# Performance work log

Hardware: AMD Instinct MI355X
Metric: run time of the kernel (lower is better)

## Reference

```python
import jax, jax.numpy as jnp
import numpy as np

ALPHA = 0.5
EPS = 1e-10

def setup_inputs() -> dict:
    key = jax.random.key(0)
    k1, k2, k3, k4 = jax.random.split(key, 4)
    B, S, H = 8, 2048, 768
    query_embs = jax.random.normal(k1, (B, S, H), dtype=jnp.float32)
    key_embs = jax.random.normal(k2, (B, S, H), dtype=jnp.float32)
    q_mask = (jax.random.uniform(k3, (B, S)) > 0.1).astype(jnp.float32)
    k_mask = (jax.random.uniform(k4, (B, S)) > 0.1).astype(jnp.float32)
    q_mask = q_mask.at[:, 0].set(1.0)
    k_mask = k_mask.at[:, 0].set(1.0)
    return {"query_embs": query_embs, "key_embs": key_embs,
            "q_mask": q_mask, "k_mask": k_mask, "gumbel_temp": 1.0}

def _l2norm(x):
    # torch F.normalize: x / max(||x||, eps-ish); use rsqrt with tiny floor
    n = jnp.sqrt(jnp.sum(x * x, axis=-1, keepdims=True))
    return x / jnp.maximum(n, 1e-12)

def reference(query_embs, key_embs, q_mask, k_mask, gumbel_temp):
    B, S, H = query_embs.shape
    q = _l2norm(query_embs)
    k = _l2norm(key_embs)
    sim = jnp.einsum('bqh,bkh->bqk', q, k)  # [B,S,S]
    # exponential distance decay w_{ij} = exp(-alpha*|i-j|)
    pos = jnp.arange(S)
    dist = jnp.abs(pos[:, None] - pos[None, :]).astype(sim.dtype)
    sim = sim * jnp.exp(-ALPHA * dist)
    valid = q_mask[:, :, None] * k_mask[:, None, :]  # [B,S,S]
    # eval path: no Gumbel noise
    noisy = sim / gumbel_temp
    noisy = noisy * valid - (1.0 - valid) * 1e9
    p = jax.nn.softmax(noisy, axis=-1)
    agg = jnp.einsum('bqk,bkh->bqh', p, k)
    scores = jnp.sum(q * agg, axis=-1) * q_mask  # [B,S]
    denom = jnp.maximum(jnp.sum(q_mask, axis=-1), 1.0)
    return jnp.sum(scores, axis=-1) / denom  # [B]
```

## Files before the change

kernel.cpp:

```cpp
#include <hip/hip_runtime.h>
#include <math.h>

#define SB 8
#define SS 2048
#define SH 768
#define ALPHA 0.5f

typedef __fp16 f16x8 __attribute__((ext_vector_type(8)));
typedef float f32x4 __attribute__((ext_vector_type(4)));

__device__ __forceinline__ float dot4(float4 a, float4 b) {
  return a.x*b.x + a.y*b.y + a.z*b.z + a.w*b.w;
}
__device__ __forceinline__ unsigned int pk2(float a, float b) {
  return __builtin_bit_cast(unsigned int, __builtin_amdgcn_cvt_pkrtz(a, b));
}
#define MFMA(a, b, c) __builtin_amdgcn_mfma_f32_16x16x32_f16(a, b, c, 0, 0, 0)


__global__ __launch_bounds__(256) void kprep_kernel(
    const float* __restrict__ K, const float* __restrict__ km,
    const float* __restrict__ qm,
    __fp16* __restrict__ Khs, float* __restrict__ ksum,
    float* __restrict__ Nk, float* __restrict__ qsum) {
  __shared__ float4 red[4][3][64];
  int b = blockIdx.y, jc = blockIdx.x, t = threadIdx.x;
  int w = t >> 6, lane = t & 63;
  int j0 = jc * 32;
  float4 acc0 = {0,0,0,0}, acc1 = {0,0,0,0}, acc2 = {0,0,0,0};
  for (int jj = 0; jj < 8; ++jj) {
    int j = j0 + 8 * w + jj;
    const float4* rp = (const float4*)(K + ((size_t)b * SS + j) * SH);
    float4 a = rp[lane], b4 = rp[lane + 64], c4 = rp[lane + 128];
    float ssv = dot4(a, a) + dot4(b4, b4) + dot4(c4, c4);
    #pragma unroll
    for (int m = 1; m < 64; m <<= 1) ssv += __shfl_xor(ssv, m, 64);
    float kwj = km[b * SS + j] / fmaxf(sqrtf(ssv), 1e-12f);
    uint2* kr = (uint2*)(Khs + ((size_t)b * SS + j) * SH);
    kr[lane]       = make_uint2(pk2(a.x*kwj,  a.y*kwj),  pk2(a.z*kwj,  a.w*kwj));
    kr[lane + 64]  = make_uint2(pk2(b4.x*kwj, b4.y*kwj), pk2(b4.z*kwj, b4.w*kwj));
    kr[lane + 128] = make_uint2(pk2(c4.x*kwj, c4.y*kwj), pk2(c4.z*kwj, c4.w*kwj));
    acc0.x += a.x*kwj;  acc0.y += a.y*kwj;  acc0.z += a.z*kwj;  acc0.w += a.w*kwj;
    acc1.x += b4.x*kwj; acc1.y += b4.y*kwj; acc1.z += b4.z*kwj; acc1.w += b4.w*kwj;
    acc2.x += c4.x*kwj; acc2.y += c4.y*kwj; acc2.z += c4.z*kwj; acc2.w += c4.w*kwj;
  }
  red[w][0][lane] = acc0; red[w][1][lane] = acc1; red[w][2][lane] = acc2;
  __syncthreads();
  if (t < 192) {
    int s = t >> 6, l = t & 63;
    float4 r0 = red[0][s][l], r1 = red[1][s][l], r2 = red[2][s][l], r3 = red[3][s][l];
    float* kp = ksum + b * SH + (s * 64 + l) * 4;
    atomicAdd(kp + 0, r0.x+r1.x+r2.x+r3.x);
    atomicAdd(kp + 1, r0.y+r1.y+r2.y+r3.y);
    atomicAdd(kp + 2, r0.z+r1.z+r2.z+r3.z);
    atomicAdd(kp + 3, r0.w+r1.w+r2.w+r3.w);
  }
  if (t < 32) {
    float pkm = km[b * SS + j0 + t];
    float pqm = qm[b * SS + j0 + t];
    #pragma unroll
    for (int m = 1; m < 32; m <<= 1) {
      pkm += __shfl_xor(pkm, m, 64);
      pqm += __shfl_xor(pqm, m, 64);
    }
    if (t == 0) { atomicAdd(&Nk[b], pkm); atomicAdd(&qsum[b], pqm); }
  }
}

__global__ __launch_bounds__(512, 1) void band_kernel(
    const float* __restrict__ Q, const __fp16* __restrict__ Khs,
    const float* __restrict__ temp, const float* __restrict__ qm,
    const float* __restrict__ ksum, const float* __restrict__ Nkp,
    const float* __restrict__ qsum,
    float* __restrict__ acc, int* __restrict__ cnt, float* __restrict__ out) {
  __shared__ f32x4 sPc[4][5][64];
  __shared__ float sSS[8][16], sDD[8][16];
  __shared__ float tab_s[64];
  int tid = threadIdx.x;
  int w = tid >> 6, lane = tid & 63;
  int l15 = lane & 15, quad = lane >> 4;
  int blk = blockIdx.x;
  int work = (blk & 7) * 128 + (blk >> 3);
  int b = work >> 7;
  int i0 = (work & 127) * 16;

  if (tid < 64) {
    float invt = 1.0f / temp[0];
    tab_s[tid] = __expf(-ALPHA * fabsf((float)(tid - 31))) * invt;
  }
  float nk = Nkp[b];
  float qm0 = qm[b * SS + i0 + quad * 4 + 0];
  float qm1 = qm[b * SS + i0 + quad * 4 + 1];
  float qm2 = qm[b * SS + i0 + quad * 4 + 2];
  float qm3 = qm[b * SS + i0 + quad * 4 + 3];

  const float* qp = Q + ((size_t)b * SS + i0 + l15) * SH + w * 96 + quad * 8;
  const float* kp = ksum + (size_t)b * SH + w * 96 + quad * 8;
  float4 x0 = *(const float4*)(qp + 0),  x1 = *(const float4*)(qp + 4);
  float4 x2 = *(const float4*)(qp + 32), x3 = *(const float4*)(qp + 36);
  float4 x4 = *(const float4*)(qp + 64), x5 = *(const float4*)(qp + 68);
  float4 g0 = *(const float4*)(kp + 0),  g1 = *(const float4*)(kp + 4);
  float4 g2 = *(const float4*)(kp + 32), g3 = *(const float4*)(kp + 36);
  float4 g4 = *(const float4*)(kp + 64), g5 = *(const float4*)(kp + 68);
  float ss = dot4(x0,x0) + dot4(x1,x1) + dot4(x2,x2)
           + dot4(x3,x3) + dot4(x4,x4) + dot4(x5,x5);
  float dd = dot4(x0,g0) + dot4(x1,g1) + dot4(x2,g2)
           + dot4(x3,g3) + dot4(x4,g4) + dot4(x5,g5);
  #define MKA(a, xA, xB) do { \
    uint4 u_ = make_uint4(pk2(xA.x, xA.y), pk2(xA.z, xA.w), \
                          pk2(xB.x, xB.y), pk2(xB.z, xB.w)); \
    a = __builtin_bit_cast(f16x8, u_); } while (0)
  f16x8 a0, a1, a2;
  MKA(a0, x0, x1); MKA(a1, x2, x3); MKA(a2, x4, x5);
  ss += __shfl_xor(ss, 16, 64); ss += __shfl_xor(ss, 32, 64);
  dd += __shfl_xor(dd, 16, 64); dd += __shfl_xor(dd, 32, 64);
  if (quad == 0) { sSS[w][l15] = ss; sDD[w][l15] = dd; }

  const __fp16* KbH = Khs + (size_t)b * SS * SH;
  f32x4 d0t, d1t, d2t, d3t, d4t;
  #define DOTILE(DT, T) do { \
    int jc_ = min(max(i0 - 32 + 16 * (T) + l15, 0), SS - 1); \
    const __fp16* bp_ = KbH + (size_t)jc_ * SH + w * 96 + quad * 8; \
    f16x8 b0_ = *(const f16x8*)(bp_); \
    f16x8 b1_ = *(const f16x8*)(bp_ + 32); \
    f16x8 b2_ = *(const f16x8*)(bp_ + 64); \
    f32x4 d_ = {0,0,0,0}; \
    d_ = MFMA(a0, b0_, d_); d_ = MFMA(a1, b1_, d_); d_ = MFMA(a2, b2_, d_); \
    DT = d_; } while (0)
  DOTILE(d0t, 0); DOTILE(d1t, 1); DOTILE(d2t, 2); DOTILE(d3t, 3); DOTILE(d4t, 4);

  if (w < 4) {
    sPc[w][0][lane] = d0t; sPc[w][1][lane] = d1t; sPc[w][2][lane] = d2t;
    sPc[w][3][lane] = d3t; sPc[w][4][lane] = d4t;
  }
  __syncthreads();
  if (w >= 4) {
    sPc[w-4][0][lane] += d0t; sPc[w-4][1][lane] += d1t;
    sPc[w-4][2][lane] += d2t; sPc[w-4][3][lane] += d3t;
    sPc[w-4][4][lane] += d4t;
  }
  __syncthreads();

  float qws[4], d0s[4];
  float qmr[4] = {qm0, qm1, qm2, qm3};
  #pragma unroll
  for (int reg = 0; reg < 4; ++reg) {
    int r = quad * 4 + reg;
    float ssr = 0.f, ddr = 0.f;
    #pragma unroll
    for (int k = 0; k < 8; ++k) { ssr += sSS[k][r]; ddr += sDD[k][r]; }
    qws[reg] = qmr[reg] / fmaxf(sqrtf(ssr), 1e-12f);
    d0s[reg] = ddr;
  }
  float an[4] = {0,0,0,0}, ad[4] = {0,0,0,0};
  #pragma unroll
  for (int t = 0; t < 5; ++t) {
    f32x4 v = sPc[0][t][lane] + sPc[1][t][lane]
            + sPc[2][t][lane] + sPc[3][t][lane];
    int j = i0 - 32 + 16 * t + l15;
    float vmask = ((unsigned)j < SS) ? 1.0f : 0.0f;
    int idxb = 16 * t + l15 - 1;
    #pragma unroll
    for (int reg = 0; reg < 4; ++reg) {
      float sv = v[reg] * qws[reg];
      int idx = min(max(idxb - quad * 4 - reg, 0), 63);
      float ev = (__expf(sv * tab_s[idx]) - 1.0f) * vmask;
      an[reg] += ev * sv;
      ad[reg] += ev;
    }
  }
  float tot = 0.f;
  #pragma unroll
  for (int reg = 0; reg < 4; ++reg) {
    float a = an[reg], e = ad[reg];
    a += __shfl_xor(a, 1, 64); a += __shfl_xor(a, 2, 64);
    a += __shfl_xor(a, 4, 64); a += __shfl_xor(a, 8, 64);
    e += __shfl_xor(e, 1, 64); e += __shfl_xor(e, 2, 64);
    e += __shfl_xor(e, 4, 64); e += __shfl_xor(e, 8, 64);
    tot += (qws[reg] * d0s[reg] + a) / (nk + e);
  }
  tot += __shfl_xor(tot, 16, 64);
  tot += __shfl_xor(tot, 32, 64);
  if (tid == 0) {
    atomicAdd(&acc[b], tot);
    __threadfence();
    if (atomicAdd(&cnt[b], 1) == 127) {
      float a2 = atomicAdd(&acc[b], 0.0f);
      out[b] = a2 / fmaxf(qsum[b], 1.0f);
    }
  }
}

extern "C" void kernel_launch(void* const* d_in, const int* in_sizes, int n_in,
                              void* d_out, int out_size, void* d_ws, size_t ws_size,
                              hipStream_t stream) {
  const float* Q    = (const float*)d_in[0];
  const float* K    = (const float*)d_in[1];
  const float* qm   = (const float*)d_in[2];
  const float* km   = (const float*)d_in[3];
  const float* temp = (const float*)d_in[4];
  float* outp = (float*)d_out;

  const size_t KHS_BYTES = (size_t)SB * SS * SH * 2;
  __fp16* Khs = (__fp16*)d_ws;
  float* ksum = (float*)((char*)d_ws + KHS_BYTES);
  float* Nk   = ksum + SB * SH;
  float* qsum = Nk + 8;
  float* accb = qsum + 8;
  int*   cnt  = (int*)(accb + 8);

  (void)hipMemsetAsync(ksum, 0, (SB * SH + 32) * sizeof(float), stream);

  kprep_kernel<<<dim3(64, SB), 256, 0, stream>>>(K, km, qm, Khs, ksum, Nk, qsum);
  band_kernel<<<1024, 512, 0, stream>>>(Q, Khs, temp, qm, ksum, Nk,
                                        qsum, accb, cnt, outp);
}
```

Baseline: 181.9 us.

## Stage banded K tiles through LDS with async double-buffered loads

The band kernel now runs 256 threads with 4 waves instead of 512 threads with 8. It stages each 16-row K tile into XOR-swizzled LDS through global_load_lds, double-buffered so the next stage's loads overlap the MFMAs on the current one. Each wave now handles 192 hidden columns with 6 MFMAs per tile, which removes the cross-wave partial-sum merge. The prep kernel now has each wave load 4 K rows at once for more memory-level parallelism, and runs twice as many blocks. The cost is more explicit barriers and waitcnt handling, plus tighter coupling to the LDS layout.

```diff
diff --git a/kernel.cpp b/kernel.cpp
--- a/kernel.cpp
+++ b/kernel.cpp
@@ -15,7 +15,16 @@
 __device__ __forceinline__ unsigned int pk2(float a, float b) {
   return __builtin_bit_cast(unsigned int, __builtin_amdgcn_cvt_pkrtz(a, b));
 }
+__device__ __forceinline__ void gl_lds16(const void* g, void* l) {
+  __builtin_amdgcn_global_load_lds(
+      (__attribute__((address_space(1))) void*)g,
+      (__attribute__((address_space(3))) void*)l, 16, 0, 0);
+}
 #define MFMA(a, b, c) __builtin_amdgcn_mfma_f32_16x16x32_f16(a, b, c, 0, 0, 0)
+#define WAITV(n) asm volatile("s_waitcnt vmcnt(" #n ")" ::: "memory")
+#define WAITL() asm volatile("s_waitcnt lgkmcnt(0)" ::: "memory")
+#define SB0() __builtin_amdgcn_sched_barrier(0)
+#define BARR() do { SB0(); __builtin_amdgcn_s_barrier(); SB0(); } while (0)
 
 
 __global__ __launch_bounds__(256) void kprep_kernel(
@@ -24,26 +33,52 @@
     __fp16* __restrict__ Khs, float* __restrict__ ksum,
     float* __restrict__ Nk, float* __restrict__ qsum) {
   __shared__ float4 red[4][3][64];
-  int b = blockIdx.y, jc = blockIdx.x, t = threadIdx.x;
+  int b = blockIdx.y, t = threadIdx.x;
   int w = t >> 6, lane = t & 63;
-  int j0 = jc * 32;
-  float4 acc0 = {0,0,0,0}, acc1 = {0,0,0,0}, acc2 = {0,0,0,0};
-  for (int jj = 0; jj < 8; ++jj) {
-    int j = j0 + 8 * w + jj;
-    const float4* rp = (const float4*)(K + ((size_t)b * SS + j) * SH);
-    float4 a = rp[lane], b4 = rp[lane + 64], c4 = rp[lane + 128];
-    float ssv = dot4(a, a) + dot4(b4, b4) + dot4(c4, c4);
-    #pragma unroll
-    for (int m = 1; m < 64; m <<= 1) ssv += __shfl_xor(ssv, m, 64);
-    float kwj = km[b * SS + j] / fmaxf(sqrtf(ssv), 1e-12f);
-    uint2* kr = (uint2*)(Khs + ((size_t)b * SS + j) * SH);
-    kr[lane]       = make_uint2(pk2(a.x*kwj,  a.y*kwj),  pk2(a.z*kwj,  a.w*kwj));
-    kr[lane + 64]  = make_uint2(pk2(b4.x*kwj, b4.y*kwj), pk2(b4.z*kwj, b4.w*kwj));
-    kr[lane + 128] = make_uint2(pk2(c4.x*kwj, c4.y*kwj), pk2(c4.z*kwj, c4.w*kwj));
-    acc0.x += a.x*kwj;  acc0.y += a.y*kwj;  acc0.z += a.z*kwj;  acc0.w += a.w*kwj;
-    acc1.x += b4.x*kwj; acc1.y += b4.y*kwj; acc1.z += b4.z*kwj; acc1.w += b4.w*kwj;
-    acc2.x += c4.x*kwj; acc2.y += c4.y*kwj; acc2.z += c4.z*kwj; acc2.w += c4.w*kwj;
-  }
+  int j0 = blockIdx.x * 16;
+  int jr = j0 + w * 4;
+  const float4* rp0 = (const float4*)(K + ((size_t)b * SS + jr + 0) * SH);
+  const float4* rp1 = (const float4*)(K + ((size_t)b * SS + jr + 1) * SH);
+  const float4* rp2 = (const float4*)(K + ((size_t)b * SS + jr + 2) * SH);
+  const float4* rp3 = (const float4*)(K + ((size_t)b * SS + jr + 3) * SH);
+  float4 A0 = rp0[lane], A1 = rp0[lane + 64], A2 = rp0[lane + 128];
+  float4 B0 = rp1[lane], B1 = rp1[lane + 64], B2 = rp1[lane + 128];
+  float4 C0 = rp2[lane], C1 = rp2[lane + 64], C2 = rp2[lane + 128];
+  float4 D0 = rp3[lane], D1 = rp3[lane + 64], D2 = rp3[lane + 128];
+  float s0 = dot4(A0,A0) + dot4(A1,A1) + dot4(A2,A2);
+  float s1 = dot4(B0,B0) + dot4(B1,B1) + dot4(B2,B2);
+  float s2 = dot4(C0,C0) + dot4(C1,C1) + dot4(C2,C2);
+  float s3 = dot4(D0,D0) + dot4(D1,D1) + dot4(D2,D2);
+  #pragma unroll
+  for (int m = 1; m < 64; m <<= 1) {
+    s0 += __shfl_xor(s0, m, 64); s1 += __shfl_xor(s1, m, 64);
+    s2 += __shfl_xor(s2, m, 64); s3 += __shfl_xor(s3, m, 64);
+  }
+  float kw0 = km[b * SS + jr + 0] / fmaxf(sqrtf(s0), 1e-12f);
+  float kw1 = km[b * SS + jr + 1] / fmaxf(sqrtf(s1), 1e-12f);
+  float kw2 = km[b * SS + jr + 2] / fmaxf(sqrtf(s2), 1e-12f);
+  float kw3 = km[b * SS + jr + 3] / fmaxf(sqrtf(s3), 1e-12f);
+  #define KST(rp, V0, V1, V2, KW, ROW) do { \
+    uint2* kr_ = (uint2*)(Khs + ((size_t)b * SS + jr + (ROW)) * SH); \
+    kr_[lane]       = make_uint2(pk2(V0.x*KW, V0.y*KW), pk2(V0.z*KW, V0.w*KW)); \
+    kr_[lane + 64]  = make_uint2(pk2(V1.x*KW, V1.y*KW), pk2(V1.z*KW, V1.w*KW)); \
+    kr_[lane + 128] = make_uint2(pk2(V2.x*KW, V2.y*KW), pk2(V2.z*KW, V2.w*KW)); \
+  } while (0)
+  KST(rp0, A0, A1, A2, kw0, 0); KST(rp1, B0, B1, B2, kw1, 1);
+  KST(rp2, C0, C1, C2, kw2, 2); KST(rp3, D0, D1, D2, kw3, 3);
+  float4 acc0, acc1, acc2;
+  acc0.x = A0.x*kw0 + B0.x*kw1 + C0.x*kw2 + D0.x*kw3;
+  acc0.y = A0.y*kw0 + B0.y*kw1 + C0.y*kw2 + D0.y*kw3;
+  acc0.z = A0.z*kw0 + B0.z*kw1 + C0.z*kw2 + D0.z*kw3;
+  acc0.w = A0.w*kw0 + B0.w*kw1 + C0.w*kw2 + D0.w*kw3;
+  acc1.x = A1.x*kw0 + B1.x*kw1 + C1.x*kw2 + D1.x*kw3;
+  acc1.y = A1.y*kw0 + B1.y*kw1 + C1.y*kw2 + D1.y*kw3;
+  acc1.z = A1.z*kw0 + B1.z*kw1 + C1.z*kw2 + D1.z*kw3;
+  acc1.w = A1.w*kw0 + B1.w*kw1 + C1.w*kw2 + D1.w*kw3;
+  acc2.x = A2.x*kw0 + B2.x*kw1 + C2.x*kw2 + D2.x*kw3;
+  acc2.y = A2.y*kw0 + B2.y*kw1 + C2.y*kw2 + D2.y*kw3;
+  acc2.z = A2.z*kw0 + B2.z*kw1 + C2.z*kw2 + D2.z*kw3;
+  acc2.w = A2.w*kw0 + B2.w*kw1 + C2.w*kw2 + D2.w*kw3;
   red[w][0][lane] = acc0; red[w][1][lane] = acc1; red[w][2][lane] = acc2;
   __syncthreads();
   if (t < 192) {
@@ -55,11 +90,11 @@
     atomicAdd(kp + 2, r0.z+r1.z+r2.z+r3.z);
     atomicAdd(kp + 3, r0.w+r1.w+r2.w+r3.w);
   }
-  if (t < 32) {
+  if (t < 16) {
     float pkm = km[b * SS + j0 + t];
     float pqm = qm[b * SS + j0 + t];
     #pragma unroll
-    for (int m = 1; m < 32; m <<= 1) {
+    for (int m = 1; m < 16; m <<= 1) {
       pkm += __shfl_xor(pkm, m, 64);
       pqm += __shfl_xor(pqm, m, 64);
     }
@@ -67,14 +102,17 @@
   }
 }
 
-__global__ __launch_bounds__(512, 1) void band_kernel(
+__global__ __launch_bounds__(256)
+__attribute__((amdgpu_waves_per_eu(2)))
+void band_kernel(
     const float* __restrict__ Q, const __fp16* __restrict__ Khs,
     const float* __restrict__ temp, const float* __restrict__ qm,
     const float* __restrict__ ksum, const float* __restrict__ Nkp,
     const float* __restrict__ qsum,
     float* __restrict__ acc, int* __restrict__ cnt, float* __restrict__ out) {
-  __shared__ f32x4 sPc[4][5][64];
-  __shared__ float sSS[8][16], sDD[8][16];
+  __shared__ __fp16 kst[2 * 12288];
+  __shared__ f32x4 sP[4][5][64];
+  __shared__ float sSS[4][16], sDD[4][16];
   __shared__ float tab_s[64];
   int tid = threadIdx.x;
   int w = tid >> 6, lane = tid & 63;
@@ -94,69 +132,95 @@
   float qm2 = qm[b * SS + i0 + quad * 4 + 2];
   float qm3 = qm[b * SS + i0 + quad * 4 + 3];
 
-  const float* qp = Q + ((size_t)b * SS + i0 + l15) * SH + w * 96 + quad * 8;
-  const float* kp = ksum + (size_t)b * SH + w * 96 + quad * 8;
-  float4 x0 = *(const float4*)(qp + 0),  x1 = *(const float4*)(qp + 4);
-  float4 x2 = *(const float4*)(qp + 32), x3 = *(const float4*)(qp + 36);
-  float4 x4 = *(const float4*)(qp + 64), x5 = *(const float4*)(qp + 68);
-  float4 g0 = *(const float4*)(kp + 0),  g1 = *(const float4*)(kp + 4);
-  float4 g2 = *(const float4*)(kp + 32), g3 = *(const float4*)(kp + 36);
-  float4 g4 = *(const float4*)(kp + 64), g5 = *(const float4*)(kp + 68);
-  float ss = dot4(x0,x0) + dot4(x1,x1) + dot4(x2,x2)
-           + dot4(x3,x3) + dot4(x4,x4) + dot4(x5,x5);
-  float dd = dot4(x0,g0) + dot4(x1,g1) + dot4(x2,g2)
-           + dot4(x3,g3) + dot4(x4,g4) + dot4(x5,g5);
-  #define MKA(a, xA, xB) do { \
-    uint4 u_ = make_uint4(pk2(xA.x, xA.y), pk2(xA.z, xA.w), \
-                          pk2(xB.x, xB.y), pk2(xB.z, xB.w)); \
-    a = __builtin_bit_cast(f16x8, u_); } while (0)
-  f16x8 a0, a1, a2;
-  MKA(a0, x0, x1); MKA(a1, x2, x3); MKA(a2, x4, x5);
+  int r0_, r1_, r2_, r3_, r4_, r5_;
+  int c0_, c1_, c2_, c3_, c4_, c5_;
+  {
+    #define PREP(u, RR, CC) do { \
+      int d_ = (u) * 4096 + tid * 16; \
+      RR = d_ / 1536; \
+      int cc_ = d_ - RR * 1536; \
+      CC = cc_ ^ ((RR & 7) << 4); } while (0)
+    PREP(0, r0_, c0_); PREP(1, r1_, c1_); PREP(2, r2_, c2_);
+    PREP(3, r3_, c3_); PREP(4, r4_, c4_); PREP(5, r5_, c5_);
+  }
+  const char* KbB = (const char*)(Khs + (size_t)b * SS * SH);
+  char* ldsb = (char*)kst;
+  #define ISSUE_STAGE(c) do { \
+    int jlo_ = i0 - 32 + 16 * (c); \
+    char* bb_ = ldsb + ((c) & 1) * 24576 + (w << 10); \
+    gl_lds16(KbB + (size_t)min(max(jlo_ + r0_, 0), SS - 1) * 1536 + c0_, bb_ + 0 * 4096); \
+    gl_lds16(KbB + (size_t)min(max(jlo_ + r1_, 0), SS - 1) * 1536 + c1_, bb_ + 1 * 4096); \
+    gl_lds16(KbB + (size_t)min(max(jlo_ + r2_, 0), SS - 1) * 1536 + c2_, bb_ + 2 * 4096); \
+    gl_lds16(KbB + (size_t)min(max(jlo_ + r3_, 0), SS - 1) * 1536 + c3_, bb_ + 3 * 4096); \
+    gl_lds16(KbB + (size_t)min(max(jlo_ + r4_, 0), SS - 1) * 1536 + c4_, bb_ + 4 * 4096); \
+    gl_lds16(KbB + (size_t)min(max(jlo_ + r5_, 0), SS - 1) * 1536 + c5_, bb_ + 5 * 4096); \
+  } while (0)
+
+  const float* qp = Q + ((size_t)b * SS + i0 + l15) * SH + w * 192 + quad * 8;
+  const float* kp = ksum + (size_t)b * SH + w * 192 + quad * 8;
+  f16x8 a0_, a1_, a2_, a3_, a4_, a5_;
+  float ss = 0.f, dd = 0.f;
+  #define PSLICE(s, A) do { \
+    float4 xa = *(const float4*)(qp + 32 * (s)); \
+    float4 xb = *(const float4*)(qp + 32 * (s) + 4); \
+    float4 ga = *(const float4*)(kp + 32 * (s)); \
+    float4 gb = *(const float4*)(kp + 32 * (s) + 4); \
+    ss += dot4(xa, xa) + dot4(xb, xb); \
+    dd += dot4(xa, ga) + dot4(xb, gb); \
+    uint4 u_ = make_uint4(pk2(xa.x, xa.y), pk2(xa.z, xa.w), \
+                          pk2(xb.x, xb.y), pk2(xb.z, xb.w)); \
+    A = __builtin_bit_cast(f16x8, u_); } while (0)
+  PSLICE(0, a0_); PSLICE(1, a1_); PSLICE(2, a2_);
+  PSLICE(3, a3_); PSLICE(4, a4_); PSLICE(5, a5_);
+
+  ISSUE_STAGE(0); ISSUE_STAGE(1);
+
   ss += __shfl_xor(ss, 16, 64); ss += __shfl_xor(ss, 32, 64);
   dd += __shfl_xor(dd, 16, 64); dd += __shfl_xor(dd, 32, 64);
   if (quad == 0) { sSS[w][l15] = ss; sDD[w][l15] = dd; }
 
-  const __fp16* KbH = Khs + (size_t)b * SS * SH;
-  f32x4 d0t, d1t, d2t, d3t, d4t;
-  #define DOTILE(DT, T) do { \
-    int jc_ = min(max(i0 - 32 + 16 * (T) + l15, 0), SS - 1); \
-    const __fp16* bp_ = KbH + (size_t)jc_ * SH + w * 96 + quad * 8; \
-    f16x8 b0_ = *(const f16x8*)(bp_); \
-    f16x8 b1_ = *(const f16x8*)(bp_ + 32); \
-    f16x8 b2_ = *(const f16x8*)(bp_ + 64); \
-    f32x4 d_ = {0,0,0,0}; \
-    d_ = MFMA(a0, b0_, d_); d_ = MFMA(a1, b1_, d_); d_ = MFMA(a2, b2_, d_); \
-    DT = d_; } while (0)
-  DOTILE(d0t, 0); DOTILE(d1t, 1); DOTILE(d2t, 2); DOTILE(d3t, 3); DOTILE(d4t, 4);
-
-  if (w < 4) {
-    sPc[w][0][lane] = d0t; sPc[w][1][lane] = d1t; sPc[w][2][lane] = d2t;
-    sPc[w][3][lane] = d3t; sPc[w][4][lane] = d4t;
-  }
-  __syncthreads();
-  if (w >= 4) {
-    sPc[w-4][0][lane] += d0t; sPc[w-4][1][lane] += d1t;
-    sPc[w-4][2][lane] += d2t; sPc[w-4][3][lane] += d3t;
-    sPc[w-4][4][lane] += d4t;
-  }
-  __syncthreads();
+  int o0_, o1_, o2_, o3_, o4_, o5_;
+  {
+    #define RPREP(s, OO) OO = l15 * 1536 + (((w * 384) + (s) * 64 + quad * 16) ^ ((l15 & 7) << 4))
+    RPREP(0, o0_); RPREP(1, o1_); RPREP(2, o2_);
+    RPREP(3, o3_); RPREP(4, o4_); RPREP(5, o5_);
+  }
+  #define DOCHUNK(c) do { \
+    const char* tb_ = ldsb + ((c) & 1) * 24576; \
+    f16x8 b0_ = *(const f16x8*)(tb_ + o0_); \
+    f16x8 b1_ = *(const f16x8*)(tb_ + o1_); \
+    f16x8 b2_ = *(const f16x8*)(tb_ + o2_); \
+    f16x8 b3_ = *(const f16x8*)(tb_ + o3_); \
+    f16x8 b4_ = *(const f16x8*)(tb_ + o4_); \
+    f16x8 b5_ = *(const f16x8*)(tb_ + o5_); \
+    f32x4 d_ = {0, 0, 0, 0}; \
+    d_ = MFMA(a0_, b0_, d_); d_ = MFMA(a1_, b1_, d_); \
+    d_ = MFMA(a2_, b2_, d_); d_ = MFMA(a3_, b3_, d_); \
+    d_ = MFMA(a4_, b4_, d_); d_ = MFMA(a5_, b5_, d_); \
+    sP[w][c][lane] = d_; } while (0)
+
+  WAITV(6); BARR(); DOCHUNK(0); BARR(); ISSUE_STAGE(2);
+  WAITV(6); BARR(); DOCHUNK(1); BARR(); ISSUE_STAGE(3);
+  WAITV(6); BARR(); DOCHUNK(2); BARR(); ISSUE_STAGE(4);
+  WAITV(6); BARR(); DOCHUNK(3); BARR();
+  WAITV(0); BARR(); DOCHUNK(4);
+  WAITL(); BARR();
 
   float qws[4], d0s[4];
   float qmr[4] = {qm0, qm1, qm2, qm3};
   #pragma unroll
   for (int reg = 0; reg < 4; ++reg) {
     int r = quad * 4 + reg;
-    float ssr = 0.f, ddr = 0.f;
-    #pragma unroll
-    for (int k = 0; k < 8; ++k) { ssr += sSS[k][r]; ddr += sDD[k][r]; }
+    float ssr = sSS[0][r] + sSS[1][r] + sSS[2][r] + sSS[3][r];
+    float ddr = sDD[0][r] + sDD[1][r] + sDD[2][r] + sDD[3][r];
     qws[reg] = qmr[reg] / fmaxf(sqrtf(ssr), 1e-12f);
     d0s[reg] = ddr;
   }
   float an[4] = {0,0,0,0}, ad[4] = {0,0,0,0};
   #pragma unroll
   for (int t = 0; t < 5; ++t) {
-    f32x4 v = sPc[0][t][lane] + sPc[1][t][lane]
-            + sPc[2][t][lane] + sPc[3][t][lane];
+    f32x4 v = sP[0][t][lane] + sP[1][t][lane]
+            + sP[2][t][lane] + sP[3][t][lane];
     int j = i0 - 32 + 16 * t + l15;
     float vmask = ((unsigned)j < SS) ? 1.0f : 0.0f;
     int idxb = 16 * t + l15 - 1;
@@ -211,7 +275,7 @@
 
   (void)hipMemsetAsync(ksum, 0, (SB * SH + 32) * sizeof(float), stream);
 
-  kprep_kernel<<<dim3(64, SB), 256, 0, stream>>>(K, km, qm, Khs, ksum, Nk, qsum);
-  band_kernel<<<1024, 512, 0, stream>>>(Q, Khs, temp, qm, ksum, Nk,
+  kprep_kernel<<<dim3(128, SB), 256, 0, stream>>>(K, km, qm, Khs, ksum, Nk, qsum);
+  band_kernel<<<1024, 256, 0, stream>>>(Q, Khs, temp, qm, ksum, Nk,
                                         qsum, accb, cnt, outp);
 }
```

New measurement: 187.8 us. +3.2%, slower.
